# Kernel optimization log

Hardware: AMD Instinct MI355X
Metric: run time of the kernel (lower is better)

Reference implementation:

```python
import jax, jax.numpy as jnp
import numpy as np

SE_TEMP = 0.2
BN_EPS = 1e-5

def _l2n(x):
    # F.normalize(p=2, dim=-1) with eps=1e-12 clamp on the norm
    n = jnp.linalg.norm(x, axis=-1, keepdims=True)
    return x / jnp.maximum(n, 1e-12)

def setup_inputs() -> dict:
    key = jax.random.key(0)
    k1, k2, k3, k4, k5 = jax.random.split(key, 5)
    Q, I, D = 256, 2048, 256
    return {
        "query_feats": jax.random.normal(k1, (Q, D), dtype=jnp.float32),
        "query_img_feats": jax.random.normal(k2, (Q, D), dtype=jnp.float32),
        "gallery_img_feats": jax.random.normal(k3, (I, D), dtype=jnp.float32),
        "bn_gamma": jnp.ones((D,), dtype=jnp.float32),
        "bn_beta": jnp.zeros((D,), dtype=jnp.float32),
        "bn_mean": jax.random.normal(k4, (D,), dtype=jnp.float32) * 0.1,
        "bn_var": jax.random.uniform(k5, (D,), dtype=jnp.float32, minval=0.5, maxval=1.5),
    }

def reference(query_feats, query_img_feats, gallery_img_feats, bn_gamma, bn_beta, bn_mean, bn_var):
    # GalleryFilterNetwork.get_scores, mode='combined', gfn_activation_mode='se'
    inv_std = bn_gamma / jnp.sqrt(bn_var + BN_EPS)

    def bn(x):  # eval-mode BatchNorm1d over last dim D
        return (x - bn_mean) * inv_std + bn_beta

    xq = _l2n(query_feats)        # [Q, D] normalized query box feats
    yq = _l2n(query_img_feats)    # [Q, D] normalized query scene feats
    yg = _l2n(gallery_img_feats)  # [I, D] normalized gallery scene feats

    gate = jax.nn.sigmoid(xq / SE_TEMP)           # [Q, D]
    fused_query = bn(yq * gate)                   # [Q, D]  (non-p SE fuse)
    fused_gal = bn(yg[:, None, :] * gate[None])   # [I, Q, D] (p=True SE fuse)

    # cosine similarity per (q, i) pair, then sigmoid
    scores = jax.nn.sigmoid(
        jnp.einsum('qd,iqd->qi', _l2n(fused_query), _l2n(fused_gal))
    )
    return scores  # [Q, I]
```

## Files before the change

kernel.cpp:

```cpp
#include <hip/hip_runtime.h>
#include <math.h>

#define D 256
#define Q 256
#define I 2048
#define STRIDE 264

typedef __attribute__((ext_vector_type(8))) short short8;
typedef __attribute__((ext_vector_type(4))) float floatx4;

__device__ __forceinline__ float wave_sum(float v) {
#pragma unroll
    for (int off = 1; off < 64; off <<= 1)
        v += __shfl_xor(v, off, 64);
    return v;
}

__device__ __forceinline__ float grp16_sum(float v) {
    v += __shfl_xor(v, 1, 64);
    v += __shfl_xor(v, 2, 64);
    v += __shfl_xor(v, 4, 64);
    v += __shfl_xor(v, 8, 64);
    return v;
}

__device__ __forceinline__ float sigmoidf_(float x) {
    return 1.0f / (1.0f + expf(-x));
}

__device__ __forceinline__ unsigned short f2bf(float f) {
    unsigned u = __float_as_uint(f);
    u += 0x7FFFu + ((u >> 16) & 1u);
    return (unsigned short)(u >> 16);
}

__global__ void __launch_bounds__(256)
query_prep(const float* __restrict__ qf,
           const float* __restrict__ qif,
           const float* __restrict__ gamma,
           const float* __restrict__ beta,
           const float* __restrict__ mean,
           const float* __restrict__ var,
           unsigned short* __restrict__ PB,
           unsigned short* __restrict__ WB,
           unsigned short* __restrict__ VB,
           float* __restrict__ sq,
           float* __restrict__ ccp) {
    const int t = threadIdx.x;
    const int wv = t >> 6, l = t & 63;
    const int q = blockIdx.x * 4 + wv;
    const float4* qf4  = (const float4*)qf;
    const float4* qif4 = (const float4*)qif;
    const float4* ga4  = (const float4*)gamma;
    const float4* be4  = (const float4*)beta;
    const float4* me4  = (const float4*)mean;
    const float4* va4  = (const float4*)var;

    float4 x = qf4[(size_t)q * 64 + l];
    float nx = wave_sum(x.x * x.x + x.y * x.y + x.z * x.z + x.w * x.w);
    float inx = 1.0f / fmaxf(sqrtf(nx), 1e-12f);
    float g0 = sigmoidf_(x.x * inx * 5.0f);
    float g1 = sigmoidf_(x.y * inx * 5.0f);
    float g2 = sigmoidf_(x.z * inx * 5.0f);
    float g3 = sigmoidf_(x.w * inx * 5.0f);

    float4 y = qif4[(size_t)q * 64 + l];
    float ny = wave_sum(y.x * y.x + y.y * y.y + y.z * y.z + y.w * y.w);
    float iny = 1.0f / fmaxf(sqrtf(ny), 1e-12f);

    float4 gm = ga4[l], bt = be4[l], mn = me4[l], vr = va4[l];
    float is0 = gm.x * rsqrtf(vr.x + 1e-5f);
    float is1 = gm.y * rsqrtf(vr.y + 1e-5f);
    float is2 = gm.z * rsqrtf(vr.z + 1e-5f);
    float is3 = gm.w * rsqrtf(vr.w + 1e-5f);
    float c0 = bt.x - mn.x * is0;
    float c1 = bt.y - mn.y * is1;
    float c2 = bt.z - mn.z * is2;
    float c3 = bt.w - mn.w * is3;
    float a0 = g0 * is0, a1 = g1 * is1, a2 = g2 * is2, a3 = g3 * is3;

    float f0 = y.x * iny * a0 + c0;
    float f1 = y.y * iny * a1 + c1;
    float f2 = y.z * iny * a2 + c2;
    float f3 = y.w * iny * a3 + c3;
    float nf = wave_sum(f0 * f0 + f1 * f1 + f2 * f2 + f3 * f3);
    float inf_ = 1.0f / fmaxf(sqrtf(nf), 1e-12f);
    float u0 = f0 * inf_, u1 = f1 * inf_, u2 = f2 * inf_, u3 = f3 * inf_;

    *(ushort4*)&PB[(size_t)q * D + 4 * l] =
        make_ushort4(f2bf(u0 * a0), f2bf(u1 * a1), f2bf(u2 * a2), f2bf(u3 * a3));
    *(ushort4*)&WB[(size_t)q * D + 4 * l] =
        make_ushort4(f2bf(a0 * a0), f2bf(a1 * a1), f2bf(a2 * a2), f2bf(a3 * a3));
    *(ushort4*)&VB[(size_t)q * D + 4 * l] =
        make_ushort4(f2bf(2.0f * a0 * c0), f2bf(2.0f * a1 * c1),
                     f2bf(2.0f * a2 * c2), f2bf(2.0f * a3 * c3));

    float s = wave_sum(u0 * c0 + u1 * c1 + u2 * c2 + u3 * c3);
    if (l == 0) sq[q] = s;

    if (q == 0) {
        float ccs = wave_sum(c0 * c0 + c1 * c1 + c2 * c2 + c3 * c3);
        if (l == 0) *ccp = ccs;
    }
}

__global__ void __launch_bounds__(256)
main_scores(const float* __restrict__ gal,
            const unsigned short* __restrict__ PB,
            const unsigned short* __restrict__ WB,
            const unsigned short* __restrict__ VB,
            const float* __restrict__ sq,
            const float* __restrict__ ccp,
            float* __restrict__ out) {
    __shared__ unsigned short sY[32 * STRIDE];
    __shared__ unsigned short sY2[32 * STRIDE];

    const int t = threadIdx.x, wv = t >> 6, l = t & 63;
    const int jq = l >> 4, s = l & 15;
    const int q0 = blockIdx.x * 64, i0 = blockIdx.y * 32;

    const float4* g4 = (const float4*)gal;
    float gx[2][16];
#pragma unroll
    for (int rr = 0; rr < 2; rr++) {
        const int i = i0 + wv * 8 + rr * 4 + jq;
#pragma unroll
        for (int m = 0; m < 4; m++) {
            float4 r = g4[(size_t)i * 64 + s * 4 + m];
            gx[rr][4 * m + 0] = r.x; gx[rr][4 * m + 1] = r.y;
            gx[rr][4 * m + 2] = r.z; gx[rr][4 * m + 3] = r.w;
        }
    }
#pragma unroll
    for (int rr = 0; rr < 2; rr++) {
        const int iloc = wv * 8 + rr * 4 + jq;
        float nn = 0.f;
#pragma unroll
        for (int e = 0; e < 16; e++) nn += gx[rr][e] * gx[rr][e];
        nn = grp16_sum(nn);
        const float inv = 1.0f / fmaxf(sqrtf(nn), 1e-12f);
        unsigned short uy[16], uy2[16];
#pragma unroll
        for (int e = 0; e < 16; e++) {
            float yv = gx[rr][e] * inv;
            uy[e]  = f2bf(yv);
            uy2[e] = f2bf(yv * yv);
        }
        *(short8*)&sY [iloc * STRIDE + s * 16]     = *(short8*)&uy[0];
        *(short8*)&sY [iloc * STRIDE + s * 16 + 8] = *(short8*)&uy[8];
        *(short8*)&sY2[iloc * STRIDE + s * 16]     = *(short8*)&uy2[0];
        *(short8*)&sY2[iloc * STRIDE + s * 16 + 8] = *(short8*)&uy2[8];
    }

    const int lm = l & 15, quad = l >> 4, koff = quad * 8;
    const int qr = q0 + wv * 16 + lm;
    short8 bp[8], bw[8], bv[8];
#pragma unroll
    for (int ks = 0; ks < 8; ks++) {
        const size_t o = (size_t)qr * D + ks * 32 + koff;
        bp[ks] = *(const short8*)&PB[o];
        bw[ks] = *(const short8*)&WB[o];
        bv[ks] = *(const short8*)&VB[o];
    }
    const float sqv = sq[qr];
    const float ccv = *ccp;

    __syncthreads();

#pragma unroll
    for (int it = 0; it < 2; it++) {
        floatx4 acc1 = {0.f, 0.f, 0.f, 0.f};
        floatx4 acc2 = {0.f, 0.f, 0.f, 0.f};
#pragma unroll
        for (int ks = 0; ks < 8; ks++) {
            const int o = (it * 16 + lm) * STRIDE + ks * 32 + koff;
            short8 ay  = *(const short8*)&sY[o];
            short8 ay2 = *(const short8*)&sY2[o];
            acc1 = __builtin_amdgcn_mfma_f32_16x16x32_bf16(ay,  bp[ks], acc1, 0, 0, 0);
            acc2 = __builtin_amdgcn_mfma_f32_16x16x32_bf16(ay2, bw[ks], acc2, 0, 0, 0);
            acc2 = __builtin_amdgcn_mfma_f32_16x16x32_bf16(ay,  bv[ks], acc2, 0, 0, 0);
        }
        float4 o4;
        float* po = &o4.x;
#pragma unroll
        for (int rr = 0; rr < 4; rr++) {
            float nrm = fmaxf(sqrtf(fmaxf(acc2[rr] + ccv, 0.f)), 1e-12f);
            po[rr] = sigmoidf_((acc1[rr] + sqv) / nrm);
        }
        *(float4*)&out[(size_t)qr * I + i0 + it * 16 + quad * 4] = o4;
    }
}

extern "C" void kernel_launch(void* const* d_in, const int* in_sizes, int n_in,
                              void* d_out, int out_size, void* d_ws, size_t ws_size,
                              hipStream_t stream) {
    const float* qf    = (const float*)d_in[0];
    const float* qif   = (const float*)d_in[1];
    const float* gal   = (const float*)d_in[2];
    const float* gamma = (const float*)d_in[3];
    const float* beta  = (const float*)d_in[4];
    const float* mean  = (const float*)d_in[5];
    const float* var   = (const float*)d_in[6];
    float* out = (float*)d_out;

    char* base = (char*)d_ws;
    float* sq = (float*)base;
    float* cc = (float*)(base + 1024);
    unsigned short* PB = (unsigned short*)(base + 2048);
    unsigned short* WB = PB + (size_t)Q * D;
    unsigned short* VB = WB + (size_t)Q * D;

    query_prep<<<Q / 4, 256, 0, stream>>>(qf, qif, gamma, beta, mean, var,
                                          PB, WB, VB, sq, cc);
    main_scores<<<dim3(Q / 64, I / 32), 256, 0, stream>>>(gal, PB, WB, VB,
                                                          sq, cc, out);
}
```

Before: 75.53 us.

## Precompute normalized gallery bf16 buffers in prep kernel; shrink main blocks to one wave

Gallery row normalization and bf16 conversion (Y and Y squared) move into the prep kernel and run once per row. Previously every q-block redid them and staged the results in LDS. The main kernel becomes a single-wave block that reads MFMA operands directly from global memory with no LDS staging or barrier. This removes redundant normalization work and LDS traffic, but raises global/L2 read redundancy of the Y buffers across q-blocks and adds a workspace round-trip.

```diff
diff --git a/kernel.cpp b/kernel.cpp
--- a/kernel.cpp
+++ b/kernel.cpp
@@ -4,7 +4,6 @@
 #define D 256
 #define Q 256
 #define I 2048
-#define STRIDE 264
 
 typedef __attribute__((ext_vector_type(8))) short short8;
 typedef __attribute__((ext_vector_type(4))) float floatx4;
@@ -13,14 +12,6 @@
 #pragma unroll
     for (int off = 1; off < 64; off <<= 1)
         v += __shfl_xor(v, off, 64);
-    return v;
-}
-
-__device__ __forceinline__ float grp16_sum(float v) {
-    v += __shfl_xor(v, 1, 64);
-    v += __shfl_xor(v, 2, 64);
-    v += __shfl_xor(v, 4, 64);
-    v += __shfl_xor(v, 8, 64);
     return v;
 }
 
@@ -35,19 +26,36 @@
 }
 
 __global__ void __launch_bounds__(256)
-query_prep(const float* __restrict__ qf,
-           const float* __restrict__ qif,
-           const float* __restrict__ gamma,
-           const float* __restrict__ beta,
-           const float* __restrict__ mean,
-           const float* __restrict__ var,
-           unsigned short* __restrict__ PB,
-           unsigned short* __restrict__ WB,
-           unsigned short* __restrict__ VB,
-           float* __restrict__ sq,
-           float* __restrict__ ccp) {
+prep(const float* __restrict__ qf,
+     const float* __restrict__ qif,
+     const float* __restrict__ gal,
+     const float* __restrict__ gamma,
+     const float* __restrict__ beta,
+     const float* __restrict__ mean,
+     const float* __restrict__ var,
+     unsigned short* __restrict__ PB,
+     unsigned short* __restrict__ WB,
+     unsigned short* __restrict__ VB,
+     unsigned short* __restrict__ YB,
+     unsigned short* __restrict__ Y2B,
+     float* __restrict__ sq,
+     float* __restrict__ ccp) {
     const int t = threadIdx.x;
     const int wv = t >> 6, l = t & 63;
+
+    if (blockIdx.x >= 64) {
+        const int i = (blockIdx.x - 64) * 4 + wv;
+        float4 x = ((const float4*)gal)[(size_t)i * 64 + l];
+        float n = wave_sum(x.x * x.x + x.y * x.y + x.z * x.z + x.w * x.w);
+        float inv = 1.0f / fmaxf(sqrtf(n), 1e-12f);
+        float y0 = x.x * inv, y1 = x.y * inv, y2 = x.z * inv, y3 = x.w * inv;
+        *(ushort4*)&YB[(size_t)i * D + 4 * l] =
+            make_ushort4(f2bf(y0), f2bf(y1), f2bf(y2), f2bf(y3));
+        *(ushort4*)&Y2B[(size_t)i * D + 4 * l] =
+            make_ushort4(f2bf(y0 * y0), f2bf(y1 * y1), f2bf(y2 * y2), f2bf(y3 * y3));
+        return;
+    }
+
     const int q = blockIdx.x * 4 + wv;
     const float4* qf4  = (const float4*)qf;
     const float4* qif4 = (const float4*)qif;
@@ -104,56 +112,20 @@
     }
 }
 
-__global__ void __launch_bounds__(256)
-main_scores(const float* __restrict__ gal,
+__global__ void __launch_bounds__(64)
+main_scores(const unsigned short* __restrict__ YB,
+            const unsigned short* __restrict__ Y2B,
             const unsigned short* __restrict__ PB,
             const unsigned short* __restrict__ WB,
             const unsigned short* __restrict__ VB,
             const float* __restrict__ sq,
             const float* __restrict__ ccp,
             float* __restrict__ out) {
-    __shared__ unsigned short sY[32 * STRIDE];
-    __shared__ unsigned short sY2[32 * STRIDE];
+    const int l = threadIdx.x;
+    const int lm = l & 15, quad = l >> 4, koff = quad * 8;
+    const int q0 = blockIdx.x * 16, i0 = blockIdx.y * 32;
+    const int qr = q0 + lm;
 
-    const int t = threadIdx.x, wv = t >> 6, l = t & 63;
-    const int jq = l >> 4, s = l & 15;
-    const int q0 = blockIdx.x * 64, i0 = blockIdx.y * 32;
-
-    const float4* g4 = (const float4*)gal;
-    float gx[2][16];
-#pragma unroll
-    for (int rr = 0; rr < 2; rr++) {
-        const int i = i0 + wv * 8 + rr * 4 + jq;
-#pragma unroll
-        for (int m = 0; m < 4; m++) {
-            float4 r = g4[(size_t)i * 64 + s * 4 + m];
-            gx[rr][4 * m + 0] = r.x; gx[rr][4 * m + 1] = r.y;
-            gx[rr][4 * m + 2] = r.z; gx[rr][4 * m + 3] = r.w;
-        }
-    }
-#pragma unroll
-    for (int rr = 0; rr < 2; rr++) {
-        const int iloc = wv * 8 + rr * 4 + jq;
-        float nn = 0.f;
-#pragma unroll
-        for (int e = 0; e < 16; e++) nn += gx[rr][e] * gx[rr][e];
-        nn = grp16_sum(nn);
-        const float inv = 1.0f / fmaxf(sqrtf(nn), 1e-12f);
-        unsigned short uy[16], uy2[16];
-#pragma unroll
-        for (int e = 0; e < 16; e++) {
-            float yv = gx[rr][e] * inv;
-            uy[e]  = f2bf(yv);
-            uy2[e] = f2bf(yv * yv);
-        }
-        *(short8*)&sY [iloc * STRIDE + s * 16]     = *(short8*)&uy[0];
-        *(short8*)&sY [iloc * STRIDE + s * 16 + 8] = *(short8*)&uy[8];
-        *(short8*)&sY2[iloc * STRIDE + s * 16]     = *(short8*)&uy2[0];
-        *(short8*)&sY2[iloc * STRIDE + s * 16 + 8] = *(short8*)&uy2[8];
-    }
-
-    const int lm = l & 15, quad = l >> 4, koff = quad * 8;
-    const int qr = q0 + wv * 16 + lm;
     short8 bp[8], bw[8], bv[8];
 #pragma unroll
     for (int ks = 0; ks < 8; ks++) {
@@ -165,17 +137,16 @@
     const float sqv = sq[qr];
     const float ccv = *ccp;
 
-    __syncthreads();
-
 #pragma unroll
     for (int it = 0; it < 2; it++) {
+        const int ir = i0 + it * 16 + lm;
         floatx4 acc1 = {0.f, 0.f, 0.f, 0.f};
         floatx4 acc2 = {0.f, 0.f, 0.f, 0.f};
 #pragma unroll
         for (int ks = 0; ks < 8; ks++) {
-            const int o = (it * 16 + lm) * STRIDE + ks * 32 + koff;
-            short8 ay  = *(const short8*)&sY[o];
-            short8 ay2 = *(const short8*)&sY2[o];
+            const size_t o = (size_t)ir * D + ks * 32 + koff;
+            short8 ay  = *(const short8*)&YB[o];
+            short8 ay2 = *(const short8*)&Y2B[o];
             acc1 = __builtin_amdgcn_mfma_f32_16x16x32_bf16(ay,  bp[ks], acc1, 0, 0, 0);
             acc2 = __builtin_amdgcn_mfma_f32_16x16x32_bf16(ay2, bw[ks], acc2, 0, 0, 0);
             acc2 = __builtin_amdgcn_mfma_f32_16x16x32_bf16(ay,  bv[ks], acc2, 0, 0, 0);
@@ -209,9 +180,11 @@
     unsigned short* PB = (unsigned short*)(base + 2048);
     unsigned short* WB = PB + (size_t)Q * D;
     unsigned short* VB = WB + (size_t)Q * D;
+    unsigned short* YB = VB + (size_t)Q * D;
+    unsigned short* Y2B = YB + (size_t)I * D;
 
-    query_prep<<<Q / 4, 256, 0, stream>>>(qf, qif, gamma, beta, mean, var,
-                                          PB, WB, VB, sq, cc);
-    main_scores<<<dim3(Q / 64, I / 32), 256, 0, stream>>>(gal, PB, WB, VB,
-                                                          sq, cc, out);
+    prep<<<576, 256, 0, stream>>>(qf, qif, gal, gamma, beta, mean, var,
+                                  PB, WB, VB, YB, Y2B, sq, cc);
+    main_scores<<<dim3(Q / 16, I / 32), 64, 0, stream>>>(YB, Y2B, PB, WB, VB,
+                                                         sq, cc, out);
 }
```

New measurement: 78.09 us. 1.03x slower.
